# Kernel optimization log

Hardware: AMD Instinct MI355X
Metric: run time of the kernel (lower is better)

## Reference

```python
import jax, jax.numpy as jnp
import numpy as np

GRID_SIZE = 5
SPLINE_ORDER = 3
ALPHA = 0.2


def _make_grid(in_features, dtype=jnp.float32):
    # uniform grid on [-1, 1] extended by spline_order on each side
    h = 2.0 / GRID_SIZE
    pts = jnp.arange(-SPLINE_ORDER, GRID_SIZE + SPLINE_ORDER + 1, dtype=dtype) * h - 1.0
    return jnp.broadcast_to(pts, (in_features, pts.shape[0]))  # [in, G+2k+1]


def _b_splines(x, grid):
    # x: [N, in] -> bases: [N, in, GRID_SIZE + SPLINE_ORDER]
    x = x[..., None]  # [N, in, 1]
    bases = ((x >= grid[:, :-1]) & (x < grid[:, 1:])).astype(x.dtype)
    for k in range(1, SPLINE_ORDER + 1):
        left = (x - grid[:, : -(k + 1)]) / (grid[:, k:-1] - grid[:, : -(k + 1)])
        right = (grid[:, k + 1 :] - x) / (grid[:, k + 1 :] - grid[:, 1:-k])
        bases = left * bases[..., :-1] + right * bases[..., 1:]
    return bases


def _kan(x, base_weight, spline_weight):
    # efficient-KAN layer: silu base linear + B-spline linear
    N, Fin = x.shape
    Fout = base_weight.shape[0]
    grid = _make_grid(Fin, x.dtype)
    bases = _b_splines(x, grid)  # [N, in, C]
    base_out = jax.nn.silu(x) @ base_weight.T
    spline_out = bases.reshape(N, -1) @ spline_weight.reshape(Fout, -1).T
    return base_out + spline_out


def setup_inputs() -> dict:
    key = jax.random.key(0)
    k1, k2, k3, k4, k5, k6 = jax.random.split(key, 6)
    N, E, Fin, Fout = 50000, 800000, 128, 128
    C = GRID_SIZE + SPLINE_ORDER
    h = jax.random.normal(k1, (N, Fin), dtype=jnp.float32)
    edge_index = jax.random.randint(k2, (2, E), 0, N, dtype=jnp.int64)
    W = jax.random.normal(k3, (Fin, Fout), dtype=jnp.float32) * (1.414 / np.sqrt(Fin))
    a = jax.random.normal(k4, (2 * Fout, 1), dtype=jnp.float32) * 0.1
    base_weight = jax.random.normal(k5, (Fout, Fin), dtype=jnp.float32) / np.sqrt(Fin)
    spline_weight = jax.random.normal(k6, (Fout, Fin, C), dtype=jnp.float32) * 0.1
    return {"h": h, "edge_index": edge_index, "W": W, "a": a,
            "base_weight": base_weight, "spline_weight": spline_weight}


def reference(h, edge_index, W, a, base_weight, spline_weight):
    N = h.shape[0]
    Fout = W.shape[1]
    HW = h @ W                                # [N, Fout]
    HW_KAN = _kan(h, base_weight, spline_weight)  # [N, Fout]
    row, col = edge_index[0], edge_index[1]
    # cat([HW_i, HW_j]) @ a == HW_i @ a[:Fout] + HW_j @ a[Fout:]; precompute per node
    s_src = HW @ a[:Fout, 0]                  # [N]
    s_dst = HW @ a[Fout:, 0]                  # [N]
    e = jax.nn.leaky_relu(s_src[row] + s_dst[col], ALPHA)  # [E]
    # segment softmax grouped by row
    m = jax.ops.segment_max(e, row, num_segments=N)
    e_exp = jnp.exp(e - m[row])
    denom = jax.ops.segment_sum(e_exp, row, num_segments=N)
    att = e_exp / denom[row]                  # [E] (dropout inactive in eval)
    out = jax.ops.segment_sum(att[:, None] * HW_KAN[col], row, num_segments=N)
    return out
```

## Files before the change

### kernel.cpp

```cpp
#include <hip/hip_runtime.h>
#include <hip/hip_bf16.h>
#include <math.h>

#define NCHUNK 9
#define BM 128
#define NTHR 512
#define PREPB ((NCHUNK * 128 * 128) / 256)

typedef __attribute__((ext_vector_type(4))) float f32x4;
typedef __attribute__((ext_vector_type(8))) short bf16x8;
typedef unsigned int u32;
typedef unsigned long long u64;

__device__ __forceinline__ unsigned short f2bf(float f) {
    u32 u = __builtin_bit_cast(u32, f);
    u32 r = (u + 0x7FFFu + ((u >> 16) & 1u)) >> 16;
    return (unsigned short)r;
}

__device__ __forceinline__ float siluf(float x) {
    return x / (1.0f + __expf(-x));
}

__global__ void k_prep(const float* __restrict__ bw, const float* __restrict__ sw,
                       const float* __restrict__ W, const float* __restrict__ a,
                       unsigned short* __restrict__ Bsw, float* __restrict__ wa,
                       const int* __restrict__ erow, int* __restrict__ counts, int E) {
    int bid = blockIdx.x;
    if (bid < PREPB) {
        int i = bid * 256 + threadIdx.x;
        int j = i & 7;
        int s = (i >> 3) & 15;
        int o = (i >> 7) & 127;
        int c = i >> 14;
        int k = c * 128 + (((s ^ (o & 7)) << 3) | j);
        float v = (k < 128) ? bw[o * 128 + k] : sw[o * 1024 + (k - 128)];
        Bsw[i] = f2bf(v);
        return;
    }
    if (bid == PREPB) {
        int fi = threadIdx.x;
        if (fi < 128) {
            float s1 = 0.f, s2 = 0.f;
            for (int o = 0; o < 128; ++o) {
                float w = W[fi * 128 + o];
                s1 = fmaf(w, a[o], s1);
                s2 = fmaf(w, a[128 + o], s2);
            }
            wa[fi] = s1;
            wa[128 + fi] = s2;
        }
        return;
    }
    int e = (bid - PREPB - 1) * 256 + threadIdx.x;
    if (e < E) atomicAdd(&counts[erow[e]], 1);
}

__global__ __launch_bounds__(NTHR) void k_nodes(const float* __restrict__ h,
                                                const unsigned short* __restrict__ Bsw,
                                                const float* __restrict__ wa,
                                                unsigned short* __restrict__ kanb,
                                                float* __restrict__ s_src,
                                                float* __restrict__ s_dst, int N, int nbn,
                                                const int* __restrict__ erow,
                                                const int* __restrict__ ecol,
                                                const int* __restrict__ offsets,
                                                int* __restrict__ cursor,
                                                int* __restrict__ colss, int E) {
    __shared__ unsigned short A_lds[BM * 128];
    __shared__ unsigned short B_lds[128 * 128];
    const int tid = threadIdx.x;

    if (blockIdx.x >= nbn) {
        int e = (blockIdx.x - nbn) * NTHR + tid;
        if (e < E) {
            int r = erow[e];
            int pos = offsets[r] + atomicAdd(&cursor[r], 1);
            colss[pos] = ecol[e];
        }
        return;
    }

    const int wid = tid >> 6, lane = tid & 63;
    const int gm0 = blockIdx.x * BM;

    const int gm = tid >> 2, gq = tid & 3;
    const float* ghr = h + (size_t)min(gm0 + gm, N - 1) * 128;

    const int wm0 = (wid >> 1) * 32;
    const int wn0 = (wid & 1) * 64;
    f32x4 acc[2][4];
#pragma unroll
    for (int im = 0; im < 2; ++im)
#pragma unroll
        for (int in = 0; in < 4; ++in) acc[im][in] = {0.f, 0.f, 0.f, 0.f};

    f32x4 pf = {0.f, 0.f, 0.f, 0.f};
    for (int chunk = 0; chunk < NCHUNK; ++chunk) {
        {
            const char* gsrc = (const char*)Bsw + (size_t)chunk * 32768 + wid * 4096 + lane * 16;
            char* ldst = (char*)B_lds + wid * 4096;
#pragma unroll
            for (int i = 0; i < 4; ++i) {
                __builtin_amdgcn_global_load_lds(
                    (const __attribute__((address_space(1))) u32*)(gsrc + i * 1024),
                    (__attribute__((address_space(3))) u32*)(ldst + i * 1024), 16, 0, 0);
            }
        }
        f32x4 pfn = pf;
        if (chunk <= 7) pfn = *(const f32x4*)(ghr + chunk * 16 + gq * 4);

        if (chunk == 0) {
            f32x4 xv[8];
#pragma unroll
            for (int v = 0; v < 8; ++v) xv[v] = *(const f32x4*)(ghr + gq * 32 + v * 4);
#pragma unroll
            for (int sl = 0; sl < 4; ++sl) {
                int s = gq * 4 + sl;
                unsigned short pk[8];
#pragma unroll
                for (int j = 0; j < 4; ++j) {
                    pk[j] = f2bf(siluf(xv[2 * sl][j]));
                    pk[4 + j] = f2bf(siluf(xv[2 * sl + 1][j]));
                }
                *(bf16x8*)((char*)A_lds + gm * 256 + (((s ^ (gm & 7)) & 15) << 4)) =
                    *(bf16x8*)pk;
            }
        } else {
#pragma unroll
            for (int j = 0; j < 4; ++j) {
                float x = pf[j];
                float t = (x + 2.2f) * 2.5f;
                float fl = floorf(t);
                int i0 = (int)fl;
                float u = t - fl;
                float um = 1.0f - u;
                float u2 = u * u, u3 = u2 * u;
                const float c6 = 1.0f / 6.0f;
                float w0 = um * um * um * c6;
                float w1 = (3.f * u3 - 6.f * u2 + 4.f) * c6;
                float w2 = (-3.f * u3 + 3.f * u2 + 3.f * u + 1.f) * c6;
                float w3 = u3 * c6;
                u64 Wp = (u64)f2bf(w0) | ((u64)f2bf(w1) << 16) |
                         ((u64)f2bf(w2) << 32) | ((u64)f2bf(w3) << 48);
                int sh = (i0 - 3) * 16;
                u64 lo = 0, hi = 0;
                if (sh >= 0) {
                    if (sh < 64) {
                        lo = Wp << sh;
                        hi = sh ? (Wp >> (64 - sh)) : 0;
                    } else if (sh < 128) {
                        hi = Wp << (sh - 64);
                    }
                } else {
                    int r = -sh;
                    if (r < 64) lo = Wp >> r;
                }
                int s = gq * 4 + j;
                ulonglong2 pv; pv.x = lo; pv.y = hi;
                *(ulonglong2*)((char*)A_lds + gm * 256 + (((s ^ (gm & 7)) & 15) << 4)) = pv;
            }
        }
        __syncthreads();

#pragma unroll
        for (int kk = 0; kk < 4; ++kk) {
            bf16x8 af[2], bfr[4];
#pragma unroll
            for (int im = 0; im < 2; ++im) {
                int mrow = wm0 + im * 16 + (lane & 15);
                int slot = (kk * 4 + (lane >> 4)) ^ (mrow & 7);
                af[im] = *(const bf16x8*)((const char*)A_lds + mrow * 256 + slot * 16);
            }
#pragma unroll
            for (int in = 0; in < 4; ++in) {
                int orow = wn0 + in * 16 + (lane & 15);
                int slot = (kk * 4 + (lane >> 4)) ^ (orow & 7);
                bfr[in] = *(const bf16x8*)((const char*)B_lds + orow * 256 + slot * 16);
            }
#pragma unroll
            for (int im = 0; im < 2; ++im)
#pragma unroll
                for (int in = 0; in < 4; ++in)
                    acc[im][in] = __builtin_amdgcn_mfma_f32_16x16x32_bf16(
                        af[im], bfr[in], acc[im][in], 0, 0, 0);
        }
        __syncthreads();
        pf = pfn;
    }

    float wa0 = wa[lane], wa1 = wa[64 + lane];
    float wa2 = wa[128 + lane], wa3 = wa[192 + lane];
    float sx0[16], sx1[16];
    const int r0 = gm0 + wid * 16;
#pragma unroll
    for (int rr = 0; rr < 16; ++rr) {
        const float* hr = h + (size_t)min(r0 + rr, N - 1) * 128;
        sx0[rr] = hr[lane];
        sx1[rr] = hr[64 + lane];
    }

#pragma unroll
    for (int im = 0; im < 2; ++im) {
        int rbase = wm0 + im * 16 + ((lane >> 4) << 2);
#pragma unroll
        for (int in = 0; in < 4; ++in) {
            int col = wn0 + in * 16 + (lane & 15);
#pragma unroll
            for (int r = 0; r < 4; ++r) {
                int row = rbase + r;
                int byte = row * 256 + ((col * 2) ^ (((row >> 2) & 3) << 5));
                *(unsigned short*)((char*)A_lds + byte) = f2bf(acc[im][in][r]);
            }
        }
    }
    __syncthreads();
    for (int i = tid; i < BM * 16; i += NTHR) {
        int row = i >> 4, s = i & 15;
        int byte = row * 256 + ((s << 4) ^ (((row >> 2) & 3) << 5));
        bf16x8 v = *(bf16x8*)((char*)A_lds + byte);
        int grow = gm0 + row;
        if (grow < N) *(bf16x8*)((char*)kanb + (size_t)grow * 256 + s * 16) = v;
    }

#pragma unroll
    for (int rr = 0; rr < 16; ++rr) {
        float s1 = fmaf(sx0[rr], wa0, sx1[rr] * wa1);
        float s2 = fmaf(sx0[rr], wa2, sx1[rr] * wa3);
#pragma unroll
        for (int off = 32; off; off >>= 1) {
            s1 += __shfl_xor(s1, off, 64);
            s2 += __shfl_xor(s2, off, 64);
        }
        int grow = r0 + rr;
        if (lane == 0 && grow < N) {
            s_src[grow] = s1;
            s_dst[grow] = s2;
        }
    }
}

__global__ void k_scan1(const int* __restrict__ counts, int* __restrict__ bsum, int N) {
    int tid = threadIdx.x;
    int idx = blockIdx.x * 256 + tid;
    int v = (idx < N) ? counts[idx] : 0;
#pragma unroll
    for (int off = 32; off; off >>= 1) v += __shfl_xor(v, off, 64);
    __shared__ int ws[4];
    if ((tid & 63) == 0) ws[tid >> 6] = v;
    __syncthreads();
    if (tid == 0) bsum[blockIdx.x] = ws[0] + ws[1] + ws[2] + ws[3];
}

__global__ __launch_bounds__(1024) void k_scan2(const int* __restrict__ bsum,
                                                int* __restrict__ ebase,
                                                int* __restrict__ offsN, int nb) {
    __shared__ int ws[16];
    __shared__ int tot;
    int tid = threadIdx.x;
    int lane = tid & 63, w = tid >> 6;
    int v = (tid < nb) ? bsum[tid] : 0;
    int inc = v;
#pragma unroll
    for (int off = 1; off < 64; off <<= 1) {
        int t = __shfl_up(inc, off, 64);
        if (lane >= off) inc += t;
    }
    if (lane == 63) ws[w] = inc;
    __syncthreads();
    if (w == 0 && lane < 16) {
        int x = ws[lane];
#pragma unroll
        for (int off = 1; off < 16; off <<= 1) {
            int t = __shfl_up(x, off, 64);
            if (lane >= off) x += t;
        }
        ws[lane] = x;
        if (lane == 15) tot = x;
    }
    __syncthreads();
    int wb = w ? ws[w - 1] : 0;
    if (tid < nb) ebase[tid] = wb + inc - v;
    if (tid == 0) offsN[0] = tot;
}

__global__ void k_scan3(const int* __restrict__ counts, const int* __restrict__ ebase,
                        int* __restrict__ offsets, int N) {
    int tid = threadIdx.x;
    int idx = blockIdx.x * 256 + tid;
    int v = (idx < N) ? counts[idx] : 0;
    int lane = tid & 63, w = tid >> 6;
    int inc = v;
#pragma unroll
    for (int off = 1; off < 64; off <<= 1) {
        int t = __shfl_up(inc, off, 64);
        if (lane >= off) inc += t;
    }
    __shared__ int ws[4];
    if (lane == 63) ws[w] = inc;
    __syncthreads();
    int wb = 0;
    for (int i = 0; i < w; ++i) wb += ws[i];
    if (idx < N) offsets[idx] = ebase[blockIdx.x] + wb + inc - v;
}

__global__ __launch_bounds__(256) void k_aggr(const int* __restrict__ offsets,
                                              int* __restrict__ cols,
                                              const float* __restrict__ s_src,
                                              const float* __restrict__ s_dst,
                                              const unsigned short* __restrict__ kanb,
                                              float* __restrict__ out, int N) {
    int wid = (blockIdx.x * 256 + threadIdx.x) >> 6;
    int lane = threadIdx.x & 63;
    if (wid >= N) return;
    int start = offsets[wid], end = offsets[wid + 1];
    int deg = end - start;
    float acc0 = 0.f, acc1 = 0.f;
    if (deg > 0) {
        float ssrc = s_src[wid];
        if (deg <= 64) {
            int key = 0x7fffffff;
            if (lane < deg) key = cols[start + lane];
#pragma unroll
            for (int k = 2; k <= 64; k <<= 1) {
#pragma unroll
                for (int j = k >> 1; j > 0; j >>= 1) {
                    int other = __shfl_xor(key, j, 64);
                    bool asc = ((lane & k) == 0);
                    bool lowr = ((lane & j) == 0);
                    int mn = min(key, other), mx = max(key, other);
                    key = (asc == lowr) ? mn : mx;
                }
            }
            float e = -3.402823466e38f;
            if (lane < deg) {
                e = ssrc + s_dst[key];
                e = (e >= 0.f) ? e : 0.2f * e;
            }
            float m = e;
#pragma unroll
            for (int off = 32; off; off >>= 1) m = fmaxf(m, __shfl_xor(m, off, 64));
            float ex = (lane < deg) ? __expf(e - m) : 0.f;
            float s = ex;
#pragma unroll
            for (int off = 32; off; off >>= 1) s += __shfl_xor(s, off, 64);
            float att = ex / s;
            u32 pbuf[8];
            float wbuf[8];
#pragma unroll
            for (int t = 0; t < 8; ++t) {
                int qc = (t < deg) ? t : 0;
                int c = __shfl(key, qc, 64);
                wbuf[t] = (t < deg) ? __shfl(att, qc, 64) : 0.f;
                pbuf[t] = ((const u32*)(kanb + (size_t)c * 128))[lane];
            }
            for (int q0 = 0; q0 < deg; q0 += 8) {
                u32 pc[8];
                float wc[8];
#pragma unroll
                for (int t = 0; t < 8; ++t) { pc[t] = pbuf[t]; wc[t] = wbuf[t]; }
                if (q0 + 8 < deg) {
#pragma unroll
                    for (int t = 0; t < 8; ++t) {
                        int q = q0 + 8 + t;
                        int qc = (q < deg) ? q : 0;
                        int c = __shfl(key, qc, 64);
                        wbuf[t] = (q < deg) ? __shfl(att, qc, 64) : 0.f;
                        pbuf[t] = ((const u32*)(kanb + (size_t)c * 128))[lane];
                    }
                }
#pragma unroll
                for (int t = 0; t < 8; ++t) {
                    float lo = __builtin_bit_cast(float, pc[t] << 16);
                    float hi = __builtin_bit_cast(float, pc[t] & 0xffff0000u);
                    acc0 = fmaf(wc[t], lo, acc0);
                    acc1 = fmaf(wc[t], hi, acc1);
                }
            }
        } else {
            if (lane == 0) {
                for (int i = start + 1; i < end; ++i) {
                    int v = cols[i];
                    int j = i - 1;
                    while (j >= start && cols[j] > v) { cols[j + 1] = cols[j]; --j; }
                    cols[j + 1] = v;
                }
            }
            __threadfence();
            float m = -3.402823466e38f;
            for (int j = start + lane; j < end; j += 64) {
                float e = ssrc + s_dst[cols[j]];
                e = (e >= 0.f) ? e : 0.2f * e;
                m = fmaxf(m, e);
            }
#pragma unroll
            for (int off = 32; off; off >>= 1) m = fmaxf(m, __shfl_xor(m, off, 64));
            float s = 0.f;
            for (int j = start + lane; j < end; j += 64) {
                float e = ssrc + s_dst[cols[j]];
                e = (e >= 0.f) ? e : 0.2f * e;
                s += __expf(e - m);
            }
#pragma unroll
            for (int off = 32; off; off >>= 1) s += __shfl_xor(s, off, 64);
            float inv = 1.0f / s;
            for (int t = start; t < end; t += 64) {
                int j = t + lane;
                float att = 0.f;
                int myc = 0;
                if (j < end) {
                    myc = cols[j];
                    float e = ssrc + s_dst[myc];
                    e = (e >= 0.f) ? e : 0.2f * e;
                    att = __expf(e - m) * inv;
                }
                int cnt = min(64, end - t);
                for (int q = 0; q < cnt; ++q) {
                    float w = __shfl(att, q, 64);
                    int c = __shfl(myc, q, 64);
                    u32 p = ((const u32*)(kanb + (size_t)c * 128))[lane];
                    float lo = __builtin_bit_cast(float, p << 16);
                    float hi = __builtin_bit_cast(float, p & 0xffff0000u);
                    acc0 = fmaf(w, lo, acc0);
                    acc1 = fmaf(w, hi, acc1);
                }
            }
        }
    }
    float2 o2 = make_float2(acc0, acc1);
    *(float2*)(out + (size_t)wid * 128 + lane * 2) = o2;
}

extern "C" void kernel_launch(void* const* d_in, const int* in_sizes, int n_in,
                              void* d_out, int out_size, void* d_ws, size_t ws_size,
                              hipStream_t stream) {
    const float* h  = (const float*)d_in[0];
    const int*   ei = (const int*)d_in[1];
    const float* W  = (const float*)d_in[2];
    const float* a  = (const float*)d_in[3];
    const float* bw = (const float*)d_in[4];
    const float* sw = (const float*)d_in[5];
    float* out = (float*)d_out;
    const int N = in_sizes[0] / 128;
    const int E = in_sizes[1] / 2;
    const int nb = (N + 255) / 256;
    const int nbn = (N + BM - 1) / BM;
    const int nbs = (E + NTHR - 1) / NTHR;
    const int nbh = (E + 255) / 256;

    char* ws = (char*)d_ws;
    auto alloc = [&](size_t bytes) {
        char* p = ws;
        ws += (bytes + 255) & ~(size_t)255;
        return p;
    };
    unsigned short* Bsw = (unsigned short*)alloc((size_t)NCHUNK * 128 * 128 * 2);
    float* wa    = (float*)alloc(256 * 4);
    float* ssrc  = (float*)alloc((size_t)N * 4);
    float* sdst  = (float*)alloc((size_t)N * 4);
    unsigned short* kanb = (unsigned short*)alloc((size_t)N * 128 * 2);
    int* counts  = (int*)alloc((size_t)N * 4);
    int* cursor  = (int*)alloc((size_t)N * 4);
    int* offsets = (int*)alloc(((size_t)N + 1) * 4);
    int* colss   = (int*)alloc((size_t)E * 4);
    int* bsum    = (int*)alloc((size_t)nb * 4);
    int* ebase   = (int*)alloc((size_t)nb * 4);

    size_t npad = ((size_t)N * 4 + 255) & ~(size_t)255;
    hipMemsetAsync(counts, 0, npad + (size_t)N * 4, stream);

    k_prep<<<PREPB + 1 + nbh, 256, 0, stream>>>(bw, sw, W, a, Bsw, wa, ei, counts, E);
    k_scan1<<<nb, 256, 0, stream>>>(counts, bsum, N);
    k_scan2<<<1, 1024, 0, stream>>>(bsum, ebase, offsets + N, nb);
    k_scan3<<<nb, 256, 0, stream>>>(counts, ebase, offsets, N);
    k_nodes<<<nbn + nbs, NTHR, 0, stream>>>(h, Bsw, wa, kanb, ssrc, sdst, N, nbn,
                                            ei, ei + E, offsets, cursor, colss, E);
    k_aggr<<<(N + 3) / 4, 256, 0, stream>>>(offsets, colss, ssrc, sdst, kanb, out, N);
}
```

Baseline: 147.9 us.

## Pre-bucket edges by row block before CSR scatter to localize writes

During the degree count pass, each edge is also appended to a coarse bucket keyed by row/64, packing the local row and column into one 32-bit word. The scatter phase in k_nodes then processes one bucket per block, so its cursor atomics and colss writes touch a small contiguous region instead of random rows across the whole graph. This adds a second global atomic per edge and an extra bucket buffer write and read. Edges are silently dropped if a bucket exceeds its fixed capacity, and packing the column into 26 bits limits the node count.

```diff
diff --git a/kernel.cpp b/kernel.cpp
--- a/kernel.cpp
+++ b/kernel.cpp
@@ -6,6 +6,7 @@
 #define BM 128
 #define NTHR 512
 #define PREPB ((NCHUNK * 128 * 128) / 256)
+#define BCAP 2048
 
 typedef __attribute__((ext_vector_type(4))) float f32x4;
 typedef __attribute__((ext_vector_type(8))) short bf16x8;
@@ -25,7 +26,9 @@
 __global__ void k_prep(const float* __restrict__ bw, const float* __restrict__ sw,
                        const float* __restrict__ W, const float* __restrict__ a,
                        unsigned short* __restrict__ Bsw, float* __restrict__ wa,
-                       const int* __restrict__ erow, int* __restrict__ counts, int E) {
+                       const int* __restrict__ erow, const int* __restrict__ ecol,
+                       int* __restrict__ counts, u32* __restrict__ bucket,
+                       int* __restrict__ bcursor, int E) {
     int bid = blockIdx.x;
     if (bid < PREPB) {
         int i = bid * 256 + threadIdx.x;
@@ -53,7 +56,15 @@
         return;
     }
     int e = (bid - PREPB - 1) * 256 + threadIdx.x;
-    if (e < E) atomicAdd(&counts[erow[e]], 1);
+    if (e < E) {
+        int r = erow[e];
+        int c = ecol[e];
+        atomicAdd(&counts[r], 1);
+        int b = r >> 6;
+        int pos = atomicAdd(&bcursor[b], 1);
+        if (pos < BCAP)
+            bucket[(size_t)b * BCAP + pos] = (u32)(r & 63) | ((u32)c << 6);
+    }
 }
 
 __global__ __launch_bounds__(NTHR) void k_nodes(const float* __restrict__ h,
@@ -62,21 +73,26 @@
                                                 unsigned short* __restrict__ kanb,
                                                 float* __restrict__ s_src,
                                                 float* __restrict__ s_dst, int N, int nbn,
-                                                const int* __restrict__ erow,
-                                                const int* __restrict__ ecol,
+                                                const u32* __restrict__ bucket,
+                                                const int* __restrict__ bcursor,
                                                 const int* __restrict__ offsets,
                                                 int* __restrict__ cursor,
-                                                int* __restrict__ colss, int E) {
+                                                int* __restrict__ colss) {
     __shared__ unsigned short A_lds[BM * 128];
     __shared__ unsigned short B_lds[128 * 128];
     const int tid = threadIdx.x;
 
     if (blockIdx.x >= nbn) {
-        int e = (blockIdx.x - nbn) * NTHR + tid;
-        if (e < E) {
-            int r = erow[e];
+        int b = blockIdx.x - nbn;
+        int base = b << 6;
+        int n = bcursor[b];
+        if (n > BCAP) n = BCAP;
+        for (int i = tid; i < n; i += NTHR) {
+            u32 pk = bucket[(size_t)b * BCAP + i];
+            int r = base | (int)(pk & 63u);
+            int c = (int)(pk >> 6);
             int pos = offsets[r] + atomicAdd(&cursor[r], 1);
-            colss[pos] = ecol[e];
+            colss[pos] = c;
         }
         return;
     }
@@ -445,8 +461,8 @@
     const int E = in_sizes[1] / 2;
     const int nb = (N + 255) / 256;
     const int nbn = (N + BM - 1) / BM;
-    const int nbs = (E + NTHR - 1) / NTHR;
-    const int nbh = (E + 255) / 256;
+    const int nbe = (E + 255) / 256;
+    const int NBUK = (N + 63) >> 6;
 
     char* ws = (char*)d_ws;
     auto alloc = [&](size_t bytes) {
@@ -461,19 +477,22 @@
     unsigned short* kanb = (unsigned short*)alloc((size_t)N * 128 * 2);
     int* counts  = (int*)alloc((size_t)N * 4);
     int* cursor  = (int*)alloc((size_t)N * 4);
+    int* bcursor = (int*)alloc((size_t)NBUK * 4);
     int* offsets = (int*)alloc(((size_t)N + 1) * 4);
     int* colss   = (int*)alloc((size_t)E * 4);
+    u32* bucket  = (u32*)alloc((size_t)NBUK * BCAP * 4);
     int* bsum    = (int*)alloc((size_t)nb * 4);
     int* ebase   = (int*)alloc((size_t)nb * 4);
 
-    size_t npad = ((size_t)N * 4 + 255) & ~(size_t)255;
-    hipMemsetAsync(counts, 0, npad + (size_t)N * 4, stream);
-
-    k_prep<<<PREPB + 1 + nbh, 256, 0, stream>>>(bw, sw, W, a, Bsw, wa, ei, counts, E);
+    size_t zlen = (size_t)((char*)(bcursor + NBUK) - (char*)counts);
+    hipMemsetAsync(counts, 0, zlen, stream);
+
+    k_prep<<<PREPB + 1 + nbe, 256, 0, stream>>>(bw, sw, W, a, Bsw, wa,
+                                                ei, ei + E, counts, bucket, bcursor, E);
     k_scan1<<<nb, 256, 0, stream>>>(counts, bsum, N);
     k_scan2<<<1, 1024, 0, stream>>>(bsum, ebase, offsets + N, nb);
     k_scan3<<<nb, 256, 0, stream>>>(counts, ebase, offsets, N);
-    k_nodes<<<nbn + nbs, NTHR, 0, stream>>>(h, Bsw, wa, kanb, ssrc, sdst, N, nbn,
-                                            ei, ei + E, offsets, cursor, colss, E);
+    k_nodes<<<nbn + NBUK, NTHR, 0, stream>>>(h, Bsw, wa, kanb, ssrc, sdst, N, nbn,
+                                             bucket, bcursor, offsets, cursor, colss);
     k_aggr<<<(N + 3) / 4, 256, 0, stream>>>(offsets, colss, ssrc, sdst, kanb, out, N);
 }
```

New measurement: 347.9 us. 2.35x slower.
